# Optimization experiments

Hardware: AMD Instinct MI355X
Metric: run time of the kernel (lower is better)

The kernel has to match this reference:

```python
import jax, jax.numpy as jnp
import numpy as np

NEG = -9e15
ALPHA = 0.2  # leaky relu slope

def setup_inputs() -> dict:
    key = jax.random.key(0)
    k1, k2, k3, k4 = jax.random.split(key, 4)
    N, Fin, Fout = 8192, 512, 256
    h = jax.random.normal(k1, (N, Fin), dtype=jnp.float32)
    adj = jax.random.randint(k2, (N, N), 0, 2, dtype=jnp.int32)
    # xavier_uniform with gain=1.414
    gain = 1.414
    limW = gain * np.sqrt(6.0 / (Fin + Fout))
    W = jax.random.uniform(k3, (Fin, Fout), dtype=jnp.float32, minval=-limW, maxval=limW)
    lima = gain * np.sqrt(6.0 / (2 * Fout + 1))
    a = jax.random.uniform(k4, (2 * Fout, 1), dtype=jnp.float32, minval=-lima, maxval=lima)
    return {"h": h, "adj": adj, "W": W, "a": a}

def reference(h, adj, W, a):
    Fout = W.shape[1]
    Wh = h @ W                                   # [N, Fout]
    # decompose a = [a1; a2]: e_ij = leaky(a1.Wh_i + a2.Wh_j)
    f1 = Wh @ a[:Fout]                           # [N, 1]
    f2 = Wh @ a[Fout:]                           # [N, 1]
    e = jax.nn.leaky_relu(f1 + f2.T, negative_slope=ALPHA)  # [N, N]
    e = jnp.where(adj > 0, e, jnp.float32(NEG))
    attention = jax.nn.softmax(e, axis=1)
    # dropout is identity at inference (training=False)
    h_prime = attention @ Wh                     # [N, Fout]
    return jax.nn.elu(h_prime)
```

## Files before the change

kernel.cpp:

```cpp
#include <hip/hip_runtime.h>
#include <cstdint>
#include <cstddef>

#define ALPHA 0.2f

typedef __attribute__((ext_vector_type(8)))  short short8;
typedef __attribute__((ext_vector_type(16))) float f32x16;

static __device__ __forceinline__ unsigned short f2bf(float x) {
  union { float f; unsigned u; } c; c.f = x;
  unsigned u = c.u;
  unsigned r = (u + 0x7FFFu + ((u >> 16) & 1u)) >> 16;
  return (unsigned short)r;
}

__global__ __launch_bounds__(256, 2) void gemm1(const float* __restrict__ h,
                                                const float* __restrict__ W,
                                                float* __restrict__ Wh) {
  __shared__ float As[32][68];
  __shared__ float Bs[32][64];
  const int t = threadIdx.x;
  const int bid = blockIdx.x;
  const int nb = bid & 3, mb = bid >> 2;
  const int m0 = mb * 64, n0 = nb * 64;
  const int ty = t >> 4, tx = t & 15;
  float acc[4][4];
#pragma unroll
  for (int i = 0; i < 4; i++)
#pragma unroll
    for (int j = 0; j < 4; j++) acc[i][j] = 0.f;

  for (int k0 = 0; k0 < 512; k0 += 32) {
#pragma unroll
    for (int c = 0; c < 2; c++) {
      int m = c * 32 + (t >> 3);
      int kq = (t & 7) * 4;
      float4 v = *(const float4*)&h[(size_t)(m0 + m) * 512 + k0 + kq];
      As[kq + 0][m] = v.x; As[kq + 1][m] = v.y;
      As[kq + 2][m] = v.z; As[kq + 3][m] = v.w;
    }
#pragma unroll
    for (int c = 0; c < 2; c++) {
      int k = c * 16 + (t >> 4);
      int n = (t & 15) * 4;
      *(float4*)&Bs[k][n] = *(const float4*)&W[(size_t)(k0 + k) * 256 + n0 + n];
    }
    __syncthreads();
#pragma unroll
    for (int k = 0; k < 32; k++) {
      float4 a = *(float4*)&As[k][ty * 4];
      float4 b = *(float4*)&Bs[k][tx * 4];
      float av[4] = {a.x, a.y, a.z, a.w};
      float bv[4] = {b.x, b.y, b.z, b.w};
#pragma unroll
      for (int i = 0; i < 4; i++)
#pragma unroll
        for (int j = 0; j < 4; j++) acc[i][j] = fmaf(av[i], bv[j], acc[i][j]);
    }
    __syncthreads();
  }
#pragma unroll
  for (int i = 0; i < 4; i++) {
    float4 v = {acc[i][0], acc[i][1], acc[i][2], acc[i][3]};
    *(float4*)&Wh[(size_t)(m0 + ty * 4 + i) * 256 + n0 + tx * 4] = v;
  }
}

__global__ __launch_bounds__(256) void rowstats(const float* __restrict__ Wh,
                                                const float* __restrict__ a,
                                                float* __restrict__ f1,
                                                float* __restrict__ f2,
                                                unsigned* __restrict__ uvpack) {
  const int t = threadIdx.x;
  const int w = t >> 6, lane = t & 63;
  const int i = blockIdx.x * 4 + w;
  float4 wv = *(const float4*)&Wh[(size_t)i * 256 + lane * 4];
  float4 a1 = *(const float4*)&a[lane * 4];
  float4 a2 = *(const float4*)&a[256 + lane * 4];
  float s1 = wv.x * a1.x + wv.y * a1.y + wv.z * a1.z + wv.w * a1.w;
  float s2 = wv.x * a2.x + wv.y * a2.y + wv.z * a2.z + wv.w * a2.w;
#pragma unroll
  for (int off = 32; off; off >>= 1) { s1 += __shfl_xor(s1, off); s2 += __shfl_xor(s2, off); }
  if (lane == 0) {
    f1[i] = s1; f2[i] = s2;
    float u = __expf(s2), v = __expf(ALPHA * s2);
    uvpack[i] = (unsigned)f2bf(u) | ((unsigned)f2bf(v) << 16);
  }
}

__global__ __launch_bounds__(256) void wtrans(const float* __restrict__ Wh,
                                              unsigned short* __restrict__ WhT) {
  __shared__ unsigned short T[64][80];
  const int t = threadIdx.x;
  const int bi = blockIdx.x & 127;
  const int bc = blockIdx.x >> 7;
  const int i0 = bi * 64, c0 = bc * 64;
  {
    const int il = t >> 2, cq = (t & 3) * 16;
#pragma unroll
    for (int k = 0; k < 4; ++k) {
      float4 v = *(const float4*)&Wh[(size_t)(i0 + il) * 256 + c0 + cq + k * 4];
      T[cq + k * 4 + 0][il] = f2bf(v.x);
      T[cq + k * 4 + 1][il] = f2bf(v.y);
      T[cq + k * 4 + 2][il] = f2bf(v.z);
      T[cq + k * 4 + 3][il] = f2bf(v.w);
    }
  }
  __syncthreads();
  {
    const int cl = t >> 2, iq = (t & 3) * 16;
    *(uint4*)&WhT[(size_t)(c0 + cl) * 8192 + i0 + iq]     = *(const uint4*)&T[cl][iq];
    *(uint4*)&WhT[(size_t)(c0 + cl) * 8192 + i0 + iq + 8] = *(const uint4*)&T[cl][iq + 8];
  }
}

__global__ __launch_bounds__(256) void f2max_k(const float* __restrict__ f2,
                                               float* __restrict__ f2maxp) {
  __shared__ float red[256];
  const int t = threadIdx.x;
  float m = -1e30f;
  for (int c = 0; c < 32; c++) m = fmaxf(m, f2[c * 256 + t]);
  red[t] = m;
  __syncthreads();
  for (int s = 128; s; s >>= 1) {
    if (t < s) red[t] = fmaxf(red[t], red[t + s]);
    __syncthreads();
  }
  if (t == 0) f2maxp[0] = red[0];
}

__global__ __launch_bounds__(256) void maskpack(const int* __restrict__ adj,
                                                unsigned long long* __restrict__ mask) {
  __shared__ unsigned long long mbuf[4][128];
  const int t = threadIdx.x, wave = t >> 6, lane = t & 63;
  const int row = blockIdx.x * 4 + wave;
  const int* ap = adj + (size_t)row * 8192 + lane;
#pragma unroll 1
  for (int it0 = 0; it0 < 128; it0 += 4) {
    int a0 = ap[(it0 + 0) * 64];
    int a1 = ap[(it0 + 1) * 64];
    int a2 = ap[(it0 + 2) * 64];
    int a3 = ap[(it0 + 3) * 64];
    unsigned long long b0 = __ballot(a0 > 0);
    unsigned long long b1 = __ballot(a1 > 0);
    unsigned long long b2 = __ballot(a2 > 0);
    unsigned long long b3 = __ballot(a3 > 0);
    if (lane == 0) {
      mbuf[wave][it0 + 0] = b0; mbuf[wave][it0 + 1] = b1;
      mbuf[wave][it0 + 2] = b2; mbuf[wave][it0 + 3] = b3;
    }
  }
  __syncthreads();
  uint4* dst = (uint4*)(mask + (size_t)blockIdx.x * 4 * 128);
  dst[t] = ((const uint4*)mbuf)[t];
}

#define ATTN_SUB(KSUB, MWORD, UCA, UCB, BFC, BFN, SCUR)                          \
  {                                                                              \
    const unsigned mbyte_ = ((MWORD) >> (((KSUB) & 1) * 16 + aselsh)) & 0xFFu;   \
    const unsigned uu_[8] = {UCA.x, UCA.y, UCA.z, UCA.w, UCB.x, UCB.y, UCB.z, UCB.w}; \
    float w_[8];                                                                 \
    _Pragma("unroll")                                                            \
    for (int jj = 0; jj < 8; jj++) {                                             \
      union { unsigned u; float f; } cu_, cv_;                                   \
      cu_.u = uu_[jj] << 16;                                                     \
      cv_.u = uu_[jj] & 0xFFFF0000u;                                             \
      float wv_ = (cu_.f > Ui) ? Ai * cu_.f : Bi * cv_.f;                        \
      int ext_ = ((int)(mbyte_ << (31 - jj))) >> 31;    \
      union { float f; int i; } wu_; wu_.f = wv_; wu_.i &= ext_;                 \
      w_[jj] = wu_.f;                                                            \
    }                                                                            \
    lpriv += ((w_[0] + w_[1]) + (w_[2] + w_[3])) + ((w_[4] + w_[5]) + (w_[6] + w_[7])); \
    union { uint4 q; short8 s; } af_;                                            \
    asm("v_cvt_pk_bf16_f32 %0, %1, %2" : "=v"(af_.q.x) : "v"(w_[0]), "v"(w_[1]));\
    asm("v_cvt_pk_bf16_f32 %0, %1, %2" : "=v"(af_.q.y) : "v"(w_[2]), "v"(w_[3]));\
    asm("v_cvt_pk_bf16_f32 %0, %1, %2" : "=v"(af_.q.z) : "v"(w_[4]), "v"(w_[5]));\
    asm("v_cvt_pk_bf16_f32 %0, %1, %2" : "=v"(af_.q.w) : "v"(w_[6]), "v"(w_[7]));\
    const int sn_ = (SCUR) + 1 < 128 ? (SCUR) + 1 : 127;                         \
    BFN[0] = *(const short8*)(wtp0 + (size_t)0 * (32 * 8192) + (size_t)sn_ * 16);\
    BFN[1] = *(const short8*)(wtp0 + (size_t)1 * (32 * 8192) + (size_t)sn_ * 16);\
    BFN[2] = *(const short8*)(wtp0 + (size_t)2 * (32 * 8192) + (size_t)sn_ * 16);\
    BFN[3] = *(const short8*)(wtp0 + (size_t)3 * (32 * 8192) + (size_t)sn_ * 16);\
    acc[0] = __builtin_amdgcn_mfma_f32_32x32x16_bf16(af_.s, BFC[0], acc[0], 0, 0, 0); \
    acc[1] = __builtin_amdgcn_mfma_f32_32x32x16_bf16(af_.s, BFC[1], acc[1], 0, 0, 0); \
    acc[2] = __builtin_amdgcn_mfma_f32_32x32x16_bf16(af_.s, BFC[2], acc[2], 0, 0, 0); \
    acc[3] = __builtin_amdgcn_mfma_f32_32x32x16_bf16(af_.s, BFC[3], acc[3], 0, 0, 0); \
  }

#define ATTN_GROUP(G, UC, UN, MC, MN)                                            \
  {                                                                              \
    const int gn_ = (G) < 31 ? (G) + 1 : 31;                                     \
    MN = mp[gn_];                                                                \
    UN[0] = *(const uint4*)(uvp + gn_ * 64 + 0);                                 \
    UN[1] = *(const uint4*)(uvp + gn_ * 64 + 4);                                 \
    ATTN_SUB(0, MC.x, UC[0], UC[1], bfA, bfB, 4 * (G) + 0);                      \
    UN[2] = *(const uint4*)(uvp + gn_ * 64 + 16);                                \
    UN[3] = *(const uint4*)(uvp + gn_ * 64 + 20);                                \
    ATTN_SUB(1, MC.x, UC[2], UC[3], bfB, bfA, 4 * (G) + 1);                      \
    UN[4] = *(const uint4*)(uvp + gn_ * 64 + 32);                                \
    UN[5] = *(const uint4*)(uvp + gn_ * 64 + 36);                                \
    ATTN_SUB(2, MC.y, UC[4], UC[5], bfA, bfB, 4 * (G) + 2);                      \
    UN[6] = *(const uint4*)(uvp + gn_ * 64 + 48);                                \
    UN[7] = *(const uint4*)(uvp + gn_ * 64 + 52);                                \
    ATTN_SUB(3, MC.y, UC[6], UC[7], bfB, bfA, 4 * (G) + 3);                      \
  }

__global__ __launch_bounds__(256, 1) void attn_main(const unsigned long long* __restrict__ maskw,
                                                    const float* __restrict__ f1,
                                                    const unsigned* __restrict__ uvpack,
                                                    const unsigned short* __restrict__ WhT,
                                                    const float* __restrict__ f2maxp,
                                                    float* __restrict__ out) {
  __shared__ float red[4][32][132];
  __shared__ float lsum[4][32];
  const int t = threadIdx.x;
  const int wave = t >> 6, lane = t & 63;
  const int jq = wave;
  const int am = lane & 31, asel = lane >> 5;
  const int aselsh = asel * 8;
  const int bid = blockIdx.x;
  const int cg = bid & 1;
  const int r0 = (bid >> 1) * 32;
  const int row = r0 + am;

  const float F2max = f2maxp[0];
  const float f1v = f1[row];
  const float x = f1v + F2max;
  const float M = x > 0.f ? x : ALPHA * x;
  const float Ai = __expf(f1v - M);
  const float Bi = __expf(ALPHA * f1v - M);
  const float Ui = __expf(-f1v);

  f32x16 acc[4] = {};
  const uint2* mp = (const uint2*)maskw + (size_t)row * 128 + jq * 32;
  const unsigned* uvp = uvpack + jq * 2048 + aselsh;
  const unsigned short* wtp0 = WhT + (size_t)(cg * 128 + am) * 8192 + jq * 2048 + aselsh;

  uint2 mg = mp[0], mgN;
  uint4 ug[8], ugN[8];
#pragma unroll
  for (int k = 0; k < 4; k++) {
    ug[2 * k]     = *(const uint4*)(uvp + k * 16);
    ug[2 * k + 1] = *(const uint4*)(uvp + k * 16 + 4);
  }
  short8 bfA[4], bfB[4];
#pragma unroll
  for (int ct = 0; ct < 4; ct++)
    bfA[ct] = *(const short8*)(wtp0 + (size_t)ct * (32 * 8192));
  float lpriv = 0.f;

#pragma unroll 1
  for (int gg = 0; gg < 16; ++gg) {
    ATTN_GROUP(2 * gg,     ug,  ugN, mg,  mgN);
    ATTN_GROUP(2 * gg + 1, ugN, ug,  mgN, mg);
  }

#pragma unroll
  for (int ct = 0; ct < 4; ct++) {
#pragma unroll
    for (int reg = 0; reg < 16; reg++) {
      const int rowl = (reg & 3) + 8 * (reg >> 2) + 4 * asel;
      red[jq][rowl][ct * 32 + am] = acc[ct][reg];
    }
  }
  lpriv += __shfl_xor(lpriv, 32);
  if (asel == 0) lsum[jq][am] = lpriv;
  __syncthreads();

  const int rr = t >> 3, cb = (t & 7) * 16;
  const float l = lsum[0][rr] + lsum[1][rr] + lsum[2][rr] + lsum[3][rr];
  const float inv = 1.0f / fmaxf(l, 1e-30f);
#pragma unroll
  for (int cc = 0; cc < 16; cc += 4) {
    float4 v;
    v.x = red[0][rr][cb + cc + 0] + red[1][rr][cb + cc + 0] + red[2][rr][cb + cc + 0] + red[3][rr][cb + cc + 0];
    v.y = red[0][rr][cb + cc + 1] + red[1][rr][cb + cc + 1] + red[2][rr][cb + cc + 1] + red[3][rr][cb + cc + 1];
    v.z = red[0][rr][cb + cc + 2] + red[1][rr][cb + cc + 2] + red[2][rr][cb + cc + 2] + red[3][rr][cb + cc + 2];
    v.w = red[0][rr][cb + cc + 3] + red[1][rr][cb + cc + 3] + red[2][rr][cb + cc + 3] + red[3][rr][cb + cc + 3];
    v.x *= inv; v.y *= inv; v.z *= inv; v.w *= inv;
    float4 o;
    o.x = v.x > 0.f ? v.x : __expf(v.x) - 1.f;
    o.y = v.y > 0.f ? v.y : __expf(v.y) - 1.f;
    o.z = v.z > 0.f ? v.z : __expf(v.z) - 1.f;
    o.w = v.w > 0.f ? v.w : __expf(v.w) - 1.f;
    *(float4*)&out[(size_t)(r0 + rr) * 256 + cg * 128 + cb + cc] = o;
  }
}

extern "C" void kernel_launch(void* const* d_in, const int* in_sizes, int n_in,
                              void* d_out, int out_size, void* d_ws, size_t ws_size,
                              hipStream_t stream) {
  const float* h  = (const float*)d_in[0];
  const int* adj  = (const int*)d_in[1];
  const float* W  = (const float*)d_in[2];
  const float* a  = (const float*)d_in[3];
  float* out = (float*)d_out;
  char* ws = (char*)d_ws;

  float* Wh            = (float*)ws;
  unsigned long long* mask = (unsigned long long*)(ws + (size_t)(8u << 20));
  unsigned short* WhT  = (unsigned short*)(ws + (size_t)(16u << 20));
  float* f1            = (float*)(ws + (size_t)(20u << 20));
  float* f2            = (float*)(ws + (size_t)(20u << 20) + (32u << 10));
  unsigned* uvpack     = (unsigned*)(ws + (size_t)(20u << 20) + (64u << 10));
  float* f2maxp        = (float*)(ws + (size_t)(20u << 20) + (96u << 10));

  maskpack<<<2048, 256, 0, stream>>>(adj, mask);
  gemm1<<<512, 256, 0, stream>>>(h, W, Wh);
  rowstats<<<2048, 256, 0, stream>>>(Wh, a, f1, f2, uvpack);
  wtrans<<<512, 256, 0, stream>>>(Wh, WhT);
  f2max_k<<<1, 256, 0, stream>>>(f2, f2maxp);
  attn_main<<<512, 256, 0, stream>>>(mask, f1, uvpack, WhT, f2maxp, out);
}
```

Measured before the change: 552.6 us.

## Merge mask packing with projection GEMM and deepen B-fragment prefetch

```diff
diff --git a/kernel.cpp b/kernel.cpp
--- a/kernel.cpp
+++ b/kernel.cpp
@@ -14,55 +14,84 @@
   return (unsigned short)r;
 }
 
-__global__ __launch_bounds__(256, 2) void gemm1(const float* __restrict__ h,
-                                                const float* __restrict__ W,
-                                                float* __restrict__ Wh) {
+__global__ __launch_bounds__(256, 2) void maskgemm(const int* __restrict__ adj,
+                                                   unsigned long long* __restrict__ mask,
+                                                   const float* __restrict__ h,
+                                                   const float* __restrict__ W,
+                                                   float* __restrict__ Wh) {
   __shared__ float As[32][68];
   __shared__ float Bs[32][64];
-  const int t = threadIdx.x;
-  const int bid = blockIdx.x;
-  const int nb = bid & 3, mb = bid >> 2;
-  const int m0 = mb * 64, n0 = nb * 64;
-  const int ty = t >> 4, tx = t & 15;
-  float acc[4][4];
-#pragma unroll
-  for (int i = 0; i < 4; i++)
-#pragma unroll
-    for (int j = 0; j < 4; j++) acc[i][j] = 0.f;
-
-  for (int k0 = 0; k0 < 512; k0 += 32) {
-#pragma unroll
-    for (int c = 0; c < 2; c++) {
-      int m = c * 32 + (t >> 3);
-      int kq = (t & 7) * 4;
-      float4 v = *(const float4*)&h[(size_t)(m0 + m) * 512 + k0 + kq];
-      As[kq + 0][m] = v.x; As[kq + 1][m] = v.y;
-      As[kq + 2][m] = v.z; As[kq + 3][m] = v.w;
-    }
-#pragma unroll
-    for (int c = 0; c < 2; c++) {
-      int k = c * 16 + (t >> 4);
-      int n = (t & 15) * 4;
-      *(float4*)&Bs[k][n] = *(const float4*)&W[(size_t)(k0 + k) * 256 + n0 + n];
+  __shared__ unsigned long long mbuf[4][128];
+  const int t = threadIdx.x;
+  const int b = blockIdx.x;
+  if (b % 5 == 0) {
+    const int bid = b / 5;
+    const int nb = bid & 3, mb = bid >> 2;
+    const int m0 = mb * 64, n0 = nb * 64;
+    const int ty = t >> 4, tx = t & 15;
+    float acc[4][4];
+#pragma unroll
+    for (int i = 0; i < 4; i++)
+#pragma unroll
+      for (int j = 0; j < 4; j++) acc[i][j] = 0.f;
+
+    for (int k0 = 0; k0 < 512; k0 += 32) {
+#pragma unroll
+      for (int c = 0; c < 2; c++) {
+        int m = c * 32 + (t >> 3);
+        int kq = (t & 7) * 4;
+        float4 v = *(const float4*)&h[(size_t)(m0 + m) * 512 + k0 + kq];
+        As[kq + 0][m] = v.x; As[kq + 1][m] = v.y;
+        As[kq + 2][m] = v.z; As[kq + 3][m] = v.w;
+      }
+#pragma unroll
+      for (int c = 0; c < 2; c++) {
+        int k = c * 16 + (t >> 4);
+        int n = (t & 15) * 4;
+        *(float4*)&Bs[k][n] = *(const float4*)&W[(size_t)(k0 + k) * 256 + n0 + n];
+      }
+      __syncthreads();
+#pragma unroll
+      for (int k = 0; k < 32; k++) {
+        float4 a = *(float4*)&As[k][ty * 4];
+        float4 bb = *(float4*)&Bs[k][tx * 4];
+        float av[4] = {a.x, a.y, a.z, a.w};
+        float bv[4] = {bb.x, bb.y, bb.z, bb.w};
+#pragma unroll
+        for (int i = 0; i < 4; i++)
+#pragma unroll
+          for (int j = 0; j < 4; j++) acc[i][j] = fmaf(av[i], bv[j], acc[i][j]);
+      }
+      __syncthreads();
+    }
+#pragma unroll
+    for (int i = 0; i < 4; i++) {
+      float4 v = {acc[i][0], acc[i][1], acc[i][2], acc[i][3]};
+      *(float4*)&Wh[(size_t)(m0 + ty * 4 + i) * 256 + n0 + tx * 4] = v;
+    }
+  } else {
+    const int mask_id = b - b / 5 - 1;
+    const int wave = t >> 6, lane = t & 63;
+    const int row = mask_id * 4 + wave;
+    const int* ap = adj + (size_t)row * 8192 + lane;
+#pragma unroll 1
+    for (int it0 = 0; it0 < 128; it0 += 4) {
+      int a0 = ap[(it0 + 0) * 64];
+      int a1 = ap[(it0 + 1) * 64];
+      int a2 = ap[(it0 + 2) * 64];
+      int a3 = ap[(it0 + 3) * 64];
+      unsigned long long b0 = __ballot(a0 > 0);
+      unsigned long long b1 = __ballot(a1 > 0);
+      unsigned long long b2 = __ballot(a2 > 0);
+      unsigned long long b3 = __ballot(a3 > 0);
+      if (lane == 0) {
+        mbuf[wave][it0 + 0] = b0; mbuf[wave][it0 + 1] = b1;
+        mbuf[wave][it0 + 2] = b2; mbuf[wave][it0 + 3] = b3;
+      }
     }
     __syncthreads();
-#pragma unroll
-    for (int k = 0; k < 32; k++) {
-      float4 a = *(float4*)&As[k][ty * 4];
-      float4 b = *(float4*)&Bs[k][tx * 4];
-      float av[4] = {a.x, a.y, a.z, a.w};
-      float bv[4] = {b.x, b.y, b.z, b.w};
-#pragma unroll
-      for (int i = 0; i < 4; i++)
-#pragma unroll
-        for (int j = 0; j < 4; j++) acc[i][j] = fmaf(av[i], bv[j], acc[i][j]);
-    }
-    __syncthreads();
-  }
-#pragma unroll
-  for (int i = 0; i < 4; i++) {
-    float4 v = {acc[i][0], acc[i][1], acc[i][2], acc[i][3]};
-    *(float4*)&Wh[(size_t)(m0 + ty * 4 + i) * 256 + n0 + tx * 4] = v;
+    uint4* dst = (uint4*)(mask + (size_t)mask_id * 4 * 128);
+    dst[t] = ((const uint4*)mbuf)[t];
   }
 }
 
@@ -129,33 +158,16 @@
   if (t == 0) f2maxp[0] = red[0];
 }
 
-__global__ __launch_bounds__(256) void maskpack(const int* __restrict__ adj,
-                                                unsigned long long* __restrict__ mask) {
-  __shared__ unsigned long long mbuf[4][128];
-  const int t = threadIdx.x, wave = t >> 6, lane = t & 63;
-  const int row = blockIdx.x * 4 + wave;
-  const int* ap = adj + (size_t)row * 8192 + lane;
-#pragma unroll 1
-  for (int it0 = 0; it0 < 128; it0 += 4) {
-    int a0 = ap[(it0 + 0) * 64];
-    int a1 = ap[(it0 + 1) * 64];
-    int a2 = ap[(it0 + 2) * 64];
-    int a3 = ap[(it0 + 3) * 64];
-    unsigned long long b0 = __ballot(a0 > 0);
-    unsigned long long b1 = __ballot(a1 > 0);
-    unsigned long long b2 = __ballot(a2 > 0);
-    unsigned long long b3 = __ballot(a3 > 0);
-    if (lane == 0) {
-      mbuf[wave][it0 + 0] = b0; mbuf[wave][it0 + 1] = b1;
-      mbuf[wave][it0 + 2] = b2; mbuf[wave][it0 + 3] = b3;
-    }
-  }
-  __syncthreads();
-  uint4* dst = (uint4*)(mask + (size_t)blockIdx.x * 4 * 128);
-  dst[t] = ((const uint4*)mbuf)[t];
-}
-
-#define ATTN_SUB(KSUB, MWORD, UCA, UCB, BFC, BFN, SCUR)                          \
+#define LOADBF(BUF, SIDX)                                                        \
+  {                                                                              \
+    const int s_ = (SIDX) < 128 ? (SIDX) : 127;                                  \
+    BUF[0] = *(const short8*)(wtp0 + (size_t)0 * (32 * 8192) + (size_t)s_ * 16); \
+    BUF[1] = *(const short8*)(wtp0 + (size_t)1 * (32 * 8192) + (size_t)s_ * 16); \
+    BUF[2] = *(const short8*)(wtp0 + (size_t)2 * (32 * 8192) + (size_t)s_ * 16); \
+    BUF[3] = *(const short8*)(wtp0 + (size_t)3 * (32 * 8192) + (size_t)s_ * 16); \
+  }
+
+#define ATTN_SUB(KSUB, MWORD, UCA, UCB, BFC)                                     \
   {                                                                              \
     const unsigned mbyte_ = ((MWORD) >> (((KSUB) & 1) * 16 + aselsh)) & 0xFFu;   \
     const unsigned uu_[8] = {UCA.x, UCA.y, UCA.z, UCA.w, UCB.x, UCB.y, UCB.z, UCB.w}; \
@@ -176,11 +188,6 @@
     asm("v_cvt_pk_bf16_f32 %0, %1, %2" : "=v"(af_.q.y) : "v"(w_[2]), "v"(w_[3]));\
     asm("v_cvt_pk_bf16_f32 %0, %1, %2" : "=v"(af_.q.z) : "v"(w_[4]), "v"(w_[5]));\
     asm("v_cvt_pk_bf16_f32 %0, %1, %2" : "=v"(af_.q.w) : "v"(w_[6]), "v"(w_[7]));\
-    const int sn_ = (SCUR) + 1 < 128 ? (SCUR) + 1 : 127;                         \
-    BFN[0] = *(const short8*)(wtp0 + (size_t)0 * (32 * 8192) + (size_t)sn_ * 16);\
-    BFN[1] = *(const short8*)(wtp0 + (size_t)1 * (32 * 8192) + (size_t)sn_ * 16);\
-    BFN[2] = *(const short8*)(wtp0 + (size_t)2 * (32 * 8192) + (size_t)sn_ * 16);\
-    BFN[3] = *(const short8*)(wtp0 + (size_t)3 * (32 * 8192) + (size_t)sn_ * 16);\
     acc[0] = __builtin_amdgcn_mfma_f32_32x32x16_bf16(af_.s, BFC[0], acc[0], 0, 0, 0); \
     acc[1] = __builtin_amdgcn_mfma_f32_32x32x16_bf16(af_.s, BFC[1], acc[1], 0, 0, 0); \
     acc[2] = __builtin_amdgcn_mfma_f32_32x32x16_bf16(af_.s, BFC[2], acc[2], 0, 0, 0); \
@@ -193,16 +200,20 @@
     MN = mp[gn_];                                                                \
     UN[0] = *(const uint4*)(uvp + gn_ * 64 + 0);                                 \
     UN[1] = *(const uint4*)(uvp + gn_ * 64 + 4);                                 \
-    ATTN_SUB(0, MC.x, UC[0], UC[1], bfA, bfB, 4 * (G) + 0);                      \
+    LOADBF(bfs2, 4 * (G) + 2);             \
+    LOADBF(bfs3, 4 * (G) + 3);                                                   \
+    ATTN_SUB(0, MC.x, UC[0], UC[1], bfs0);                                       \
     UN[2] = *(const uint4*)(uvp + gn_ * 64 + 16);                                \
     UN[3] = *(const uint4*)(uvp + gn_ * 64 + 20);                                \
-    ATTN_SUB(1, MC.x, UC[2], UC[3], bfB, bfA, 4 * (G) + 1);                      \
+    ATTN_SUB(1, MC.x, UC[2], UC[3], bfs1);                                       \
     UN[4] = *(const uint4*)(uvp + gn_ * 64 + 32);                                \
     UN[5] = *(const uint4*)(uvp + gn_ * 64 + 36);                                \
-    ATTN_SUB(2, MC.y, UC[4], UC[5], bfA, bfB, 4 * (G) + 2);                      \
+    LOADBF(bfs0, 4 * (G) + 4);             \
+    LOADBF(bfs1, 4 * (G) + 5);                                                   \
+    ATTN_SUB(2, MC.y, UC[4], UC[5], bfs2);                                       \
     UN[6] = *(const uint4*)(uvp + gn_ * 64 + 48);                                \
     UN[7] = *(const uint4*)(uvp + gn_ * 64 + 52);                                \
-    ATTN_SUB(3, MC.y, UC[6], UC[7], bfB, bfA, 4 * (G) + 3);                      \
+    ATTN_SUB(3, MC.y, UC[6], UC[7], bfs3);                                       \
   }
 
 __global__ __launch_bounds__(256, 1) void attn_main(const unsigned long long* __restrict__ maskw,
@@ -243,10 +254,9 @@
     ug[2 * k]     = *(const uint4*)(uvp + k * 16);
     ug[2 * k + 1] = *(const uint4*)(uvp + k * 16 + 4);
   }
-  short8 bfA[4], bfB[4];
-#pragma unroll
-  for (int ct = 0; ct < 4; ct++)
-    bfA[ct] = *(const short8*)(wtp0 + (size_t)ct * (32 * 8192));
+  short8 bfs0[4], bfs1[4], bfs2[4], bfs3[4];
+  LOADBF(bfs0, 0);
+  LOADBF(bfs1, 1);
   float lpriv = 0.f;
 
 #pragma unroll 1
@@ -305,8 +315,7 @@
   unsigned* uvpack     = (unsigned*)(ws + (size_t)(20u << 20) + (64u << 10));
   float* f2maxp        = (float*)(ws + (size_t)(20u << 20) + (96u << 10));
 
-  maskpack<<<2048, 256, 0, stream>>>(adj, mask);
-  gemm1<<<512, 256, 0, stream>>>(h, W, Wh);
+  maskgemm<<<2560, 256, 0, stream>>>(adj, mask, h, W, Wh);
   rowstats<<<2048, 256, 0, stream>>>(Wh, a, f1, f2, uvpack);
   wtrans<<<512, 256, 0, stream>>>(Wh, WhT);
   f2max_k<<<1, 256, 0, stream>>>(f2, f2maxp);
```

New measurement: 537.4 us. 2.7% less time.
